# Kernel tuning notes

Hardware: AMD Instinct MI355X
Metric: run time of the kernel (lower is better)

## Reference

```python
import jax, jax.numpy as jnp
import numpy as np

B, D, H, C, HALT_H, MAX_STEPS = 8192, 2048, 1024, 1000, 32, 10
EPS = 1e-08


def setup_inputs() -> dict:
    key = jax.random.key(0)
    ks = jax.random.split(key, 12)
    s = 0.02
    return {
        "x": jax.random.normal(ks[0], (B, D), jnp.float32),
        "enc_W": jax.random.normal(ks[1], (H, D), jnp.float32) * s,
        "enc_b": jnp.zeros((H,), jnp.float32),
        "ln_g": jnp.ones((H,), jnp.float32),
        "ln_b": jnp.zeros((H,), jnp.float32),
        "W_ih": jax.random.normal(ks[2], (3 * H, H), jnp.float32) * s,
        "W_hh": jax.random.normal(ks[3], (3 * H, H), jnp.float32) * s,
        "b_ih": jnp.zeros((3 * H,), jnp.float32),
        "b_hh": jnp.zeros((3 * H,), jnp.float32),
        "cls_W": jax.random.normal(ks[4], (C, H), jnp.float32) * s,
        "cls_b": jnp.zeros((C,), jnp.float32),
        "h1_W": jax.random.normal(ks[5], (HALT_H, H), jnp.float32) * s,
        "h1_b": jnp.zeros((HALT_H,), jnp.float32),
        "h2_W": jax.random.normal(ks[6], (1, HALT_H), jnp.float32) * s,
        "h2_b": jnp.zeros((1,), jnp.float32),
    }


def _forward(x, enc_W, enc_b, ln_g, ln_b, W_ih, W_hh, b_ih, b_hh,
             cls_W, cls_b, h1_W, h1_b, h2_W, h2_b):
    # encoder: Linear -> LayerNorm -> GELU (exact)
    z = x @ enc_W.T + enc_b
    mu = jnp.mean(z, axis=-1, keepdims=True)
    var = jnp.var(z, axis=-1, keepdims=True)
    z = (z - mu) * jax.lax.rsqrt(var + 1e-05) * ln_g + ln_b
    h0 = jax.nn.gelu(z, approximate=False)

    def step(h, _):
        gi = h @ W_ih.T + b_ih   # GRUCell with input = hidden
        gh = h @ W_hh.T + b_hh
        gi_r, gi_z, gi_n = jnp.split(gi, 3, axis=-1)
        gh_r, gh_z, gh_n = jnp.split(gh, 3, axis=-1)
        r = jax.nn.sigmoid(gi_r + gh_r)
        zt = jax.nn.sigmoid(gi_z + gh_z)
        n = jnp.tanh(gi_n + r * gh_n)
        h_new = (1.0 - zt) * n + zt * h
        logits = h_new @ cls_W.T + cls_b                         # [B, C]
        halt = jax.nn.sigmoid(
            jax.nn.relu(h_new @ h1_W.T + h1_b) @ h2_W.T + h2_b
        )[:, 0]                                                   # [B]
        return h_new, (logits, halt)

    _, (logits_steps, halt_steps) = jax.lax.scan(step, h0, None, length=MAX_STEPS)
    logits_stack = jnp.transpose(logits_steps, (1, 0, 2))  # [B, T, C]
    halts_stack = jnp.transpose(halt_steps, (1, 0))        # [B, T]

    log_not_halt = jnp.log(1.0 - halts_stack + EPS)
    cumsum_log = jnp.cumsum(log_not_halt, axis=1)
    cumsum_shifted = jnp.concatenate(
        [jnp.zeros((halts_stack.shape[0], 1), halts_stack.dtype), cumsum_log[:, :-1]], axis=1)
    halt_dist = halts_stack * jnp.exp(cumsum_shifted)
    remainder = 1.0 - jnp.sum(halt_dist, axis=1, keepdims=True)
    halt_dist = jnp.concatenate(
        [halt_dist[:, :-1], halt_dist[:, -1:] + jnp.maximum(remainder, 0.0)], axis=1)

    weighted_logits = jnp.sum(halt_dist[:, :, None] * logits_stack, axis=1)  # [B, C]
    step_indices = jnp.arange(1, MAX_STEPS + 1, dtype=weighted_logits.dtype)
    expected_steps = jnp.sum(halt_dist * step_indices, axis=1)
    probs = jax.nn.softmax(weighted_logits, axis=1)
    softmax_conf = jnp.max(probs, axis=1)
    comp_uncertainty = expected_steps / MAX_STEPS
    confidence = 0.7 * softmax_conf + 0.3 * (1.0 - comp_uncertainty)
    return (weighted_logits, probs, confidence, softmax_conf,
            expected_steps, halt_dist, comp_uncertainty)


def reference(x, enc_W, enc_b, ln_g, ln_b, W_ih, W_hh, b_ih, b_hh,
              cls_W, cls_b, h1_W, h1_b, h2_W, h2_b):
    return _forward(x, enc_W, enc_b, ln_g, ln_b, W_ih, W_hh, b_ih, b_hh,
                    cls_W, cls_b, h1_W, h1_b, h2_W, h2_b)
```

## Files before the change

### kernel.cpp

```cpp
#include <hip/hip_runtime.h>
#include <hip/hip_bf16.h>

#define B_ 8192
#define D_ 2048
#define H_ 1024
#define C_ 1000
#define NSTEP 10

typedef __attribute__((ext_vector_type(8))) short short8;
typedef __attribute__((ext_vector_type(4))) float f32x4;

__device__ __forceinline__ f32x4 mfma16x16(short8 a, short8 b, f32x4 c) {
  return __builtin_amdgcn_mfma_f32_16x16x32_bf16(a, b, c, 0, 0, 0);
}

__device__ __forceinline__ void async16(void* lds_uniform, const void* gsrc) {
  __builtin_amdgcn_global_load_lds(
      (const __attribute__((address_space(1))) void*)gsrc,
      (__attribute__((address_space(3))) void*)lds_uniform, 16, 0, 0);
}

__device__ __forceinline__ float sigm(float x) { return 1.0f / (1.0f + __expf(-x)); }
__device__ __forceinline__ float tanh_fast(float x) { return 1.0f - 2.0f / (__expf(2.0f * x) + 1.0f); }
__device__ __forceinline__ float b2f(short s) {
  union { unsigned u; float f; } v; v.u = ((unsigned)(unsigned short)s) << 16; return v.f;
}
__device__ __forceinline__ unsigned short f2us(float f) {
  __hip_bfloat16 h = __float2bfloat16(f); return *(unsigned short*)&h;
}

__device__ __forceinline__ int swz(int row, int slot) {
  return (row << 7) + (((slot) ^ (row & 7)) << 4);
}

__global__ void cvt_bf16_pad(const float* __restrict__ src, __hip_bfloat16* __restrict__ dst,
                             int n4, int nsrc4) {
  int i = blockIdx.x * 256 + threadIdx.x;
  if (i >= n4) return;
  float4 v = make_float4(0.f, 0.f, 0.f, 0.f);
  if (i < nsrc4) v = ((const float4*)src)[i];
  ((ushort4*)dst)[i] = make_ushort4(f2us(v.x), f2us(v.y), f2us(v.z), f2us(v.w));
}

__global__ void cvt_gates(const float* __restrict__ Wih, const float* __restrict__ Whh,
                          __hip_bfloat16* __restrict__ dst) {
  const int i = blockIdx.x * 256 + threadIdx.x;
  const int per_gate = (H_ * H_) / 4;
  const int gate = i / per_gate, rem = i - gate * per_gate;
  float4 v;
  if (gate == 0) {
    float4 a = ((const float4*)Wih)[rem], b = ((const float4*)Whh)[rem];
    v = make_float4(a.x + b.x, a.y + b.y, a.z + b.z, a.w + b.w);
  } else if (gate == 1) {
    float4 a = ((const float4*)Wih)[per_gate + rem], b = ((const float4*)Whh)[per_gate + rem];
    v = make_float4(a.x + b.x, a.y + b.y, a.z + b.z, a.w + b.w);
  } else if (gate == 2) {
    v = ((const float4*)Wih)[2 * per_gate + rem];
  } else {
    v = ((const float4*)Whh)[2 * per_gate + rem];
  }
  ((ushort4*)dst)[i] = make_ushort4(f2us(v.x), f2us(v.y), f2us(v.z), f2us(v.w));
}

template<int EPI>
__global__ __launch_bounds__(256, 2)
void gemm_bt(const __hip_bfloat16* __restrict__ A, int lda,
             const __hip_bfloat16* __restrict__ Bt, int ldb, int K,
             const float* __restrict__ bias,
             float* __restrict__ out, int out_ld, int ncol,
             const float* __restrict__ wrow) {
  __shared__ __hip_bfloat16 sA[128 * 64];
  __shared__ __hip_bfloat16 sB[128 * 64];
  const int tid = threadIdx.x;
  const int wave = tid >> 6, lane = tid & 63;
  const int m0 = blockIdx.x * 128, n0 = blockIdx.y * 128;
  const int wm = (wave >> 1) * 64, wn = (wave & 1) * 64;
  const int lr = lane & 15;
  const int g4 = lane >> 4;
  const int srow = wave * 8 + (lane >> 3);
  const int scol = ((lane & 7) ^ ((lane >> 3) & 7)) * 8;

  f32x4 acc[4][4] = {};

  const __hip_bfloat16* Asrc = A + (size_t)(m0 + srow) * lda + scol;
  const __hip_bfloat16* Bsrc = Bt + (size_t)(n0 + srow) * ldb + scol;

  for (int k0 = 0; k0 < K; k0 += 64) {
#pragma unroll
    for (int c = 0; c < 4; ++c) {
      async16((char*)sA + c * 4096 + wave * 1024, Asrc + (size_t)(c * 32) * lda + k0);
      async16((char*)sB + c * 4096 + wave * 1024, Bsrc + (size_t)(c * 32) * ldb + k0);
    }
    __syncthreads();
#pragma unroll
    for (int ks = 0; ks < 2; ++ks) {
      const int slot = ks * 4 + g4;
      short8 af[4], bfr[4];
#pragma unroll
      for (int i = 0; i < 4; ++i) {
        af[i]  = *(const short8*)((const char*)sA + swz(wm + i * 16 + lr, slot));
        bfr[i] = *(const short8*)((const char*)sB + swz(wn + i * 16 + lr, slot));
      }
#pragma unroll
      for (int i = 0; i < 4; ++i)
#pragma unroll
        for (int j = 0; j < 4; ++j)
          acc[i][j] = mfma16x16(af[i], bfr[j], acc[i][j]);
    }
    __syncthreads();
  }

  const int rbase = (lane >> 4) * 4;
  const int cbase = lane & 15;
#pragma unroll
  for (int i = 0; i < 4; ++i) {
#pragma unroll
    for (int r = 0; r < 4; ++r) {
      const int grow = m0 + wm + i * 16 + rbase + r;
      if (EPI == 1) {
        const float ws = wrow[grow];
#pragma unroll
        for (int j = 0; j < 4; ++j) {
          const int gcol = n0 + wn + j * 16 + cbase;
          if (gcol < ncol)
            out[(size_t)grow * out_ld + gcol] = acc[i][j][r] + bias[gcol] * ws;
        }
      } else {
#pragma unroll
        for (int j = 0; j < 4; ++j) {
          const int gcol = n0 + wn + j * 16 + cbase;
          out[(size_t)grow * out_ld + gcol] = acc[i][j][r] + bias[gcol];
        }
      }
    }
  }
}

__global__ __launch_bounds__(512, 1)
void gemm_gru(const __hip_bfloat16* __restrict__ A,
              const __hip_bfloat16* __restrict__ Wc4,
              const float* __restrict__ b_ih, const float* __restrict__ b_hh,
              __hip_bfloat16* __restrict__ hnewb) {
  __shared__ __align__(16) char lds[4 * 24576];
  const int tid = threadIdx.x, wave = tid >> 6, lane = tid & 63;
  const int m0 = blockIdx.x * 256, n0 = blockIdx.y * 32;
  const int wm = (wave >> 1) * 64;
  const int wc = wave & 1;
  const int lr = lane & 15, g4 = lane >> 4;
  const int soff = ((g4 ^ ((lr >> 1) & 3)) << 4);

  f32x4 acc[4][4] = {};

  const int scol = (((lane & 3) ^ ((lane >> 3) & 3)) << 3);
  const __hip_bfloat16* AsrcS = A + (size_t)(m0 + wave * 16 + (lane >> 2)) * H_ + scol;
  const __hip_bfloat16* BsrcS = Wc4 + ((size_t)(wave >> 1) << 20)
      + (size_t)(n0 + (wave & 1) * 16 + (lane >> 2)) * H_ + scol;

  auto stageA = [&](char* buf, int kt) {
#pragma unroll
    for (int c = 0; c < 2; ++c)
      async16(buf + c * 8192 + wave * 1024, AsrcS + (size_t)(c * 128) * H_ + kt * 32);
  };
  auto stageB = [&](char* buf, int kt) {
    async16(buf + 16384 + wave * 1024, BsrcS + kt * 32);
  };

  stageA(lds, 0);              stageB(lds, 0);
  stageA(lds + 24576, 1);      stageB(lds + 24576, 1);
  stageA(lds + 2 * 24576, 2);  stageB(lds + 2 * 24576, 2);
  asm volatile("s_waitcnt vmcnt(6)" ::: "memory");
  __builtin_amdgcn_s_barrier();

#pragma unroll 4
  for (int t = 0; t < 32; ++t) {
    char* rb = lds + (t & 3) * 24576;
    char* sb = lds + ((t + 3) & 3) * 24576;
    const bool dostage = (t + 3 < 32);

    short8 af[4], bf01[2];
#pragma unroll
    for (int mi = 0; mi < 4; ++mi)
      af[mi] = *(const short8*)(rb + (wm + mi * 16 + lr) * 64 + soff);
#pragma unroll
    for (int g = 0; g < 2; ++g)
      bf01[g] = *(const short8*)(rb + 16384 + g * 2048 + (wc * 16 + lr) * 64 + soff);
    if (dostage) stageA(sb, t + 3);
    __builtin_amdgcn_s_barrier();
    __builtin_amdgcn_s_setprio(1);
#pragma unroll
    for (int mi = 0; mi < 4; ++mi) {
      acc[mi][0] = mfma16x16(af[mi], bf01[0], acc[mi][0]);
      acc[mi][1] = mfma16x16(af[mi], bf01[1], acc[mi][1]);
    }
    __builtin_amdgcn_s_setprio(0);
    __builtin_amdgcn_s_barrier();

    short8 bf23[2];
#pragma unroll
    for (int g = 0; g < 2; ++g)
      bf23[g] = *(const short8*)(rb + 16384 + (2 + g) * 2048 + (wc * 16 + lr) * 64 + soff);
    if (dostage) stageB(sb, t + 3);
    __builtin_amdgcn_s_barrier();
    __builtin_amdgcn_s_setprio(1);
#pragma unroll
    for (int mi = 0; mi < 4; ++mi) {
      acc[mi][2] = mfma16x16(af[mi], bf23[0], acc[mi][2]);
      acc[mi][3] = mfma16x16(af[mi], bf23[1], acc[mi][3]);
    }
    __builtin_amdgcn_s_setprio(0);
    if (t < 29)       asm volatile("s_waitcnt vmcnt(6)" ::: "memory");
    else if (t == 29) asm volatile("s_waitcnt vmcnt(3)" ::: "memory");
    else if (t == 30) asm volatile("s_waitcnt vmcnt(0)" ::: "memory");
    __builtin_amdgcn_s_barrier();
  }

  const int rbase = (lane >> 4) * 4;
  const int cbase = lane & 15;
  const int gcol = n0 + wc * 16 + cbase;
  const float brz = b_ih[gcol] + b_hh[gcol];
  const float bzz = b_ih[H_ + gcol] + b_hh[H_ + gcol];
  const float bin = b_ih[2 * H_ + gcol];
  const float bhn = b_hh[2 * H_ + gcol];
#pragma unroll
  for (int mi = 0; mi < 4; ++mi) {
#pragma unroll
    for (int r = 0; r < 4; ++r) {
      const int grow = m0 + wm + mi * 16 + rbase + r;
      const size_t idx = (size_t)grow * H_ + gcol;
      const float rg = sigm(acc[mi][0][r] + brz);
      const float zg = sigm(acc[mi][1][r] + bzz);
      const float ng = tanh_fast(acc[mi][2][r] + bin + rg * (acc[mi][3][r] + bhn));
      const float hv = b2f(*(const short*)(A + idx));
      hnewb[idx] = __float2bfloat16((1.0f - zg) * ng + zg * hv);
    }
  }
}

__global__ void ln_gelu(const float* __restrict__ z, const float* __restrict__ g,
                        const float* __restrict__ bta, __hip_bfloat16* __restrict__ hb) {
  const int row = blockIdx.x, t = threadIdx.x;
  __shared__ float rs[4], rs2[4];
  float4 v = ((const float4*)(z + (size_t)row * H_))[t];
  float s = v.x + v.y + v.z + v.w;
  float s2 = v.x * v.x + v.y * v.y + v.z * v.z + v.w * v.w;
#pragma unroll
  for (int off = 32; off; off >>= 1) {
    s += __shfl_down(s, off);
    s2 += __shfl_down(s2, off);
  }
  if ((t & 63) == 0) { rs[t >> 6] = s; rs2[t >> 6] = s2; }
  __syncthreads();
  const float mu = (rs[0] + rs[1] + rs[2] + rs[3]) * (1.0f / H_);
  const float var = (rs2[0] + rs2[1] + rs2[2] + rs2[3]) * (1.0f / H_) - mu * mu;
  const float rstd = rsqrtf(var + 1e-5f);
  float4 gg = ((const float4*)g)[t];
  float4 bb = ((const float4*)bta)[t];
  float o[4], res[4];
  o[0] = (v.x - mu) * rstd * gg.x + bb.x;
  o[1] = (v.y - mu) * rstd * gg.y + bb.y;
  o[2] = (v.z - mu) * rstd * gg.z + bb.z;
  o[3] = (v.w - mu) * rstd * gg.w + bb.w;
#pragma unroll
  for (int k = 0; k < 4; ++k)
    res[k] = 0.5f * o[k] * (1.0f + erff(o[k] * 0.70710678118654752f));
  ((ushort4*)(hb + (size_t)row * H_))[t] =
      make_ushort4(f2us(res[0]), f2us(res[1]), f2us(res[2]), f2us(res[3]));
}

__global__ __launch_bounds__(256, 4)
void halt_mlp2(const __hip_bfloat16* __restrict__ hb,
               const __hip_bfloat16* __restrict__ h1Wb,
               const float* __restrict__ h1b, const float* __restrict__ h2W,
               const float* __restrict__ h2b,
               float* __restrict__ cum, float* __restrict__ psum,
               float* __restrict__ esum, float* __restrict__ wsum,
               float* __restrict__ out_hd, float* __restrict__ out_es,
               float* __restrict__ out_cu, int step) {
  __shared__ float part[2][2][64][8];
  const int tid = threadIdx.x, wave = tid >> 6, lane = tid & 63;
  const int rowgrp = wave >> 1, khalf = wave & 1;
  const int m0 = (blockIdx.x * 2 + rowgrp) * 16;
  const int lr = lane & 15, lk = (lane >> 4) * 8;

  const __hip_bfloat16* Arow = hb + (size_t)(m0 + lr) * H_ + khalf * 512 + lk;
  const __hip_bfloat16* B0 = h1Wb + (size_t)lr * H_ + khalf * 512 + lk;
  const __hip_bfloat16* B1 = h1Wb + (size_t)(16 + lr) * H_ + khalf * 512 + lk;
  f32x4 acc0 = {}, acc1 = {};
#pragma unroll 4
  for (int kk = 0; kk < 512; kk += 32) {
    short8 a  = *(const short8*)(Arow + kk);
    short8 b0 = *(const short8*)(B0 + kk);
    short8 b1 = *(const short8*)(B1 + kk);
    acc0 = mfma16x16(a, b0, acc0);
    acc1 = mfma16x16(a, b1, acc1);
  }
#pragma unroll
  for (int q = 0; q < 4; ++q) {
    part[rowgrp][khalf][lane][q]     = acc0[q];
    part[rowgrp][khalf][lane][4 + q] = acc1[q];
  }
  __syncthreads();
  if (khalf) return;

  const float w2a = h2W[lr], w2b = h2W[16 + lr];
  const float b1a = h1b[lr], b1b = h1b[16 + lr];
  float p[4];
#pragma unroll
  for (int q = 0; q < 4; ++q) {
    const float u0 = part[rowgrp][0][lane][q]     + part[rowgrp][1][lane][q]     + b1a;
    const float u1 = part[rowgrp][0][lane][4 + q] + part[rowgrp][1][lane][4 + q] + b1b;
    p[q] = fmaxf(u0, 0.f) * w2a + fmaxf(u1, 0.f) * w2b;
  }
#pragma unroll
  for (int m = 1; m < 16; m <<= 1) {
#pragma unroll
    for (int q = 0; q < 4; ++q) p[q] += __shfl_xor(p[q], m);
  }
  if (lr == 0) {
    const float b2 = h2b[0];
#pragma unroll
    for (int q = 0; q < 4; ++q) {
      const int rl = (lane >> 4) * 4 + q;
      const int row = m0 + rl;
      const float halt = 1.f / (1.f + expf(-(p[q] + b2)));
      float c  = (step == 0) ? 0.f : cum[row];
      float ps = (step == 0) ? 0.f : psum[row];
      float es = (step == 0) ? 0.f : esum[row];
      const float pt = halt * expf(c);
      float w;
      if (step == NSTEP - 1) {
        w = pt + fmaxf(1.f - (ps + pt), 0.f);
        es += w * (float)NSTEP;
        out_es[row] = es;
        out_cu[row] = es * (1.0f / NSTEP);
        wsum[row] = ps + w;
      } else {
        w = pt;
        es += w * (float)(step + 1);
        cum[row] = c + logf(1.f - halt + 1e-8f);
        psum[row] = ps + pt;
        esum[row] = es;
      }
      out_hd[(size_t)row * NSTEP + step] = w;
    }
  }
}

__global__ void hw_final(const __hip_bfloat16* __restrict__ hstack,
                         const float* __restrict__ out_hd,
                         __hip_bfloat16* __restrict__ hwb) {
  const int t = threadIdx.x;
  const int row = blockIdx.x * 4 + (t >> 6);
  const int c0 = (t & 63) * 16;
  const float* hd = out_hd + (size_t)row * NSTEP;
  float accv[16] = {};
#pragma unroll
  for (int s = 0; s < NSTEP; ++s) {
    const float w = hd[s];
    const short8* p = (const short8*)(hstack + ((size_t)(s + 1) * B_ + row) * H_ + c0);
    short8 a0 = p[0], a1 = p[1];
#pragma unroll
    for (int q = 0; q < 8; ++q) accv[q] += w * b2f(a0[q]);
#pragma unroll
    for (int q = 0; q < 8; ++q) accv[8 + q] += w * b2f(a1[q]);
  }
  short8 r0, r1;
#pragma unroll
  for (int q = 0; q < 8; ++q) { r0[q] = (short)f2us(accv[q]); r1[q] = (short)f2us(accv[8 + q]); }
  short8* dst = (short8*)(hwb + (size_t)row * H_ + c0);
  dst[0] = r0; dst[1] = r1;
}

__global__ void finalize(const float* __restrict__ wl, const float* __restrict__ es,
                         float* __restrict__ probs, float* __restrict__ conf,
                         float* __restrict__ sconf) {
  const int row = blockIdx.x, t = threadIdx.x;
  __shared__ float red[4], red2[4];
  float4 v = make_float4(-1e30f, -1e30f, -1e30f, -1e30f);
  float m = -1e30f;
  if (t < 250) {
    v = ((const float4*)(wl + (size_t)row * C_))[t];
    m = fmaxf(fmaxf(v.x, v.y), fmaxf(v.z, v.w));
  }
#pragma unroll
  for (int off = 32; off; off >>= 1) m = fmaxf(m, __shfl_down(m, off));
  if ((t & 63) == 0) red[t >> 6] = m;
  __syncthreads();
  m = fmaxf(fmaxf(red[0], red[1]), fmaxf(red[2], red[3]));
  float4 e = make_float4(0.f, 0.f, 0.f, 0.f);
  float s = 0.f;
  if (t < 250) {
    e.x = expf(v.x - m); e.y = expf(v.y - m); e.z = expf(v.z - m); e.w = expf(v.w - m);
    s = e.x + e.y + e.z + e.w;
  }
#pragma unroll
  for (int off = 32; off; off >>= 1) s += __shfl_down(s, off);
  if ((t & 63) == 0) red2[t >> 6] = s;
  __syncthreads();
  s = red2[0] + red2[1] + red2[2] + red2[3];
  const float inv = 1.0f / s;
  if (t < 250)
    ((float4*)(probs + (size_t)row * C_))[t] = make_float4(e.x * inv, e.y * inv, e.z * inv, e.w * inv);
  if (t == 0) {
    sconf[row] = inv;
    conf[row] = 0.7f * inv + 0.3f * (1.0f - es[row] * (1.0f / NSTEP));
  }
}

extern "C" void kernel_launch(void* const* d_in, const int* in_sizes, int n_in,
                              void* d_out, int out_size, void* d_ws, size_t ws_size,
                              hipStream_t stream) {
  (void)in_sizes; (void)n_in; (void)out_size; (void)ws_size;
  const float* x     = (const float*)d_in[0];
  const float* enc_W = (const float*)d_in[1];
  const float* enc_b = (const float*)d_in[2];
  const float* ln_g  = (const float*)d_in[3];
  const float* ln_b  = (const float*)d_in[4];
  const float* W_ih  = (const float*)d_in[5];
  const float* W_hh  = (const float*)d_in[6];
  const float* b_ih  = (const float*)d_in[7];
  const float* b_hh  = (const float*)d_in[8];
  const float* cls_W = (const float*)d_in[9];
  const float* cls_b = (const float*)d_in[10];
  const float* h1_W  = (const float*)d_in[11];
  const float* h1_b  = (const float*)d_in[12];
  const float* h2_W  = (const float*)d_in[13];
  const float* h2_b  = (const float*)d_in[14];

  char* wsp = (char*)d_ws;
  auto carve = [&](size_t n) { char* p = wsp; wsp += (n + 255) & ~(size_t)255; return p; };
  __hip_bfloat16* Wc4b   = (__hip_bfloat16*)carve((size_t)4 * H_ * H_ * 2);
  __hip_bfloat16* clsWb  = (__hip_bfloat16*)carve((size_t)1024 * 1024 * 2);
  __hip_bfloat16* encWb  = (__hip_bfloat16*)carve((size_t)H_ * D_ * 2);
  __hip_bfloat16* h1Wb   = (__hip_bfloat16*)carve((size_t)32 * H_ * 2);
  __hip_bfloat16* hstack = (__hip_bfloat16*)carve((size_t)(NSTEP + 1) * B_ * H_ * 2);
  float* cum  = (float*)carve((size_t)B_ * 4);
  float* psum = (float*)carve((size_t)B_ * 4);
  float* esum = (float*)carve((size_t)B_ * 4);
  float* wsum = (float*)carve((size_t)B_ * 4);

  const size_t SLOT = (size_t)B_ * H_;
  float* z            = (float*)(hstack + SLOT);
  __hip_bfloat16* xb  = hstack + 3 * SLOT;
  __hip_bfloat16* hwb = hstack;

  float* out = (float*)d_out;
  float* out_wl    = out;
  float* out_probs = out + (size_t)B_ * C_;
  float* out_conf  = out + (size_t)2 * B_ * C_;
  float* out_sconf = out_conf + B_;
  float* out_es    = out_sconf + B_;
  float* out_hd    = out_es + B_;
  float* out_cu    = out_hd + (size_t)B_ * NSTEP;

  dim3 blk(256);
  { int n4 = B_ * D_ / 4;       cvt_bf16_pad<<<(n4 + 255) / 256, blk, 0, stream>>>(x, xb, n4, n4); }
  { int n4 = H_ * D_ / 4;       cvt_bf16_pad<<<(n4 + 255) / 256, blk, 0, stream>>>(enc_W, encWb, n4, n4); }
  { int n4 = 4 * H_ * H_ / 4;   cvt_gates<<<(n4 + 255) / 256, blk, 0, stream>>>(W_ih, W_hh, Wc4b); }
  { int n4 = 1024 * 1024 / 4;   cvt_bf16_pad<<<(n4 + 255) / 256, blk, 0, stream>>>(cls_W, clsWb, n4, C_ * H_ / 4); }
  { int n4 = 32 * H_ / 4;       cvt_bf16_pad<<<(n4 + 255) / 256, blk, 0, stream>>>(h1_W, h1Wb, n4, n4); }

  gemm_bt<0><<<dim3(B_ / 128, H_ / 128), blk, 0, stream>>>(
      xb, D_, encWb, D_, D_, enc_b, z, H_, H_, nullptr);
  ln_gelu<<<B_, blk, 0, stream>>>(z, ln_g, ln_b, hstack);

  for (int step = 0; step < NSTEP; ++step) {
    const __hip_bfloat16* hprev = hstack + (size_t)step * SLOT;
    __hip_bfloat16* hnext = hstack + (size_t)(step + 1) * SLOT;
    gemm_gru<<<dim3(B_ / 256, H_ / 32), dim3(512), 0, stream>>>(
        hprev, Wc4b, b_ih, b_hh, hnext);
    halt_mlp2<<<B_ / 32, blk, 0, stream>>>(
        hnext, h1Wb, h1_b, h2_W, h2_b, cum, psum, esum, wsum,
        out_hd, out_es, out_cu, step);
  }

  hw_final<<<B_ / 4, blk, 0, stream>>>(hstack, out_hd, hwb);

  gemm_bt<1><<<dim3(B_ / 128, 1024 / 128), blk, 0, stream>>>(
      hwb, H_, clsWb, H_, H_, cls_b, out_wl, C_, C_, wsum);

  finalize<<<B_, blk, 0, stream>>>(out_wl, out_es, out_probs, out_conf, out_sconf);
}
```

Before: 1.082 ms.

## Widen GRU gate GEMM tile to 64 hidden columns per block

Each gemm_gru block now covers 64 hidden columns instead of 32, so every A tile loaded into LDS feeds twice as many MFMAs. The LDS stage buffer grows to 32 KB, B staging issues two loads per wave, and accumulators double to 128 floats per lane. Fragment loads are reorganised so B fragments are held across both A halves, with explicit lgkmcnt waits added. The aim is to cut A-operand global and LDS traffic, at the cost of higher register pressure and half as many blocks in the grid.

```diff
diff --git a/kernel.cpp b/kernel.cpp
--- a/kernel.cpp
+++ b/kernel.cpp
@@ -141,20 +141,21 @@
               const __hip_bfloat16* __restrict__ Wc4,
               const float* __restrict__ b_ih, const float* __restrict__ b_hh,
               __hip_bfloat16* __restrict__ hnewb) {
-  __shared__ __align__(16) char lds[4 * 24576];
+  __shared__ __align__(16) char lds[4 * 32768];
   const int tid = threadIdx.x, wave = tid >> 6, lane = tid & 63;
-  const int m0 = blockIdx.x * 256, n0 = blockIdx.y * 32;
-  const int wm = (wave >> 1) * 64;
+  const int m0 = blockIdx.x * 256, n0 = blockIdx.y * 64;
+  const int wr = wave >> 1;
   const int wc = wave & 1;
+  const int wm = wr * 64;
   const int lr = lane & 15, g4 = lane >> 4;
   const int soff = ((g4 ^ ((lr >> 1) & 3)) << 4);
 
-  f32x4 acc[4][4] = {};
+  f32x4 acc[4][4][2] = {};
 
   const int scol = (((lane & 3) ^ ((lane >> 3) & 3)) << 3);
   const __hip_bfloat16* AsrcS = A + (size_t)(m0 + wave * 16 + (lane >> 2)) * H_ + scol;
-  const __hip_bfloat16* BsrcS = Wc4 + ((size_t)(wave >> 1) << 20)
-      + (size_t)(n0 + (wave & 1) * 16 + (lane >> 2)) * H_ + scol;
+  const __hip_bfloat16* BsrcS = Wc4 + ((size_t)(wave >> 2) << 20)
+      + (size_t)(n0 + (wave & 3) * 16 + (lane >> 2)) * H_ + scol;
 
   auto stageA = [&](char* buf, int kt) {
 #pragma unroll
@@ -162,76 +163,86 @@
       async16(buf + c * 8192 + wave * 1024, AsrcS + (size_t)(c * 128) * H_ + kt * 32);
   };
   auto stageB = [&](char* buf, int kt) {
-    async16(buf + 16384 + wave * 1024, BsrcS + kt * 32);
+#pragma unroll
+    for (int d = 0; d < 2; ++d)
+      async16(buf + 16384 + d * 8192 + wave * 1024, BsrcS + ((size_t)d << 21) + kt * 32);
   };
 
   stageA(lds, 0);              stageB(lds, 0);
-  stageA(lds + 24576, 1);      stageB(lds + 24576, 1);
-  stageA(lds + 2 * 24576, 2);  stageB(lds + 2 * 24576, 2);
-  asm volatile("s_waitcnt vmcnt(6)" ::: "memory");
+  stageA(lds + 32768, 1);      stageB(lds + 32768, 1);
+  stageA(lds + 2 * 32768, 2);  stageB(lds + 2 * 32768, 2);
+  asm volatile("s_waitcnt vmcnt(8)" ::: "memory");
   __builtin_amdgcn_s_barrier();
 
 #pragma unroll 4
   for (int t = 0; t < 32; ++t) {
-    char* rb = lds + (t & 3) * 24576;
-    char* sb = lds + ((t + 3) & 3) * 24576;
-    const bool dostage = (t + 3 < 32);
-
-    short8 af[4], bf01[2];
-#pragma unroll
-    for (int mi = 0; mi < 4; ++mi)
-      af[mi] = *(const short8*)(rb + (wm + mi * 16 + lr) * 64 + soff);
-#pragma unroll
-    for (int g = 0; g < 2; ++g)
-      bf01[g] = *(const short8*)(rb + 16384 + g * 2048 + (wc * 16 + lr) * 64 + soff);
+    char* rb = lds + (t & 3) * 32768;
+    char* sb = lds + ((t + 3) & 3) * 32768;
+    const bool dostage = (t < 29);
+
+    short8 af0 = *(const short8*)(rb + (wm + 0 * 16 + lr) * 64 + soff);
+    short8 af1 = *(const short8*)(rb + (wm + 1 * 16 + lr) * 64 + soff);
+    short8 bf[4][2];
+#pragma unroll
+    for (int g = 0; g < 4; ++g)
+#pragma unroll
+      for (int hb = 0; hb < 2; ++hb)
+        bf[g][hb] = *(const short8*)(rb + 16384 + (g * 64 + wc * 32 + hb * 16 + lr) * 64 + soff);
     if (dostage) stageA(sb, t + 3);
     __builtin_amdgcn_s_barrier();
+    asm volatile("s_waitcnt lgkmcnt(0)" ::: "memory");
     __builtin_amdgcn_s_setprio(1);
 #pragma unroll
-    for (int mi = 0; mi < 4; ++mi) {
-      acc[mi][0] = mfma16x16(af[mi], bf01[0], acc[mi][0]);
-      acc[mi][1] = mfma16x16(af[mi], bf01[1], acc[mi][1]);
-    }
+    for (int g = 0; g < 4; ++g)
+#pragma unroll
+      for (int hb = 0; hb < 2; ++hb) {
+        acc[0][g][hb] = mfma16x16(af0, bf[g][hb], acc[0][g][hb]);
+        acc[1][g][hb] = mfma16x16(af1, bf[g][hb], acc[1][g][hb]);
+      }
     __builtin_amdgcn_s_setprio(0);
     __builtin_amdgcn_s_barrier();
 
-    short8 bf23[2];
-#pragma unroll
-    for (int g = 0; g < 2; ++g)
-      bf23[g] = *(const short8*)(rb + 16384 + (2 + g) * 2048 + (wc * 16 + lr) * 64 + soff);
+    short8 af2 = *(const short8*)(rb + (wm + 2 * 16 + lr) * 64 + soff);
+    short8 af3 = *(const short8*)(rb + (wm + 3 * 16 + lr) * 64 + soff);
     if (dostage) stageB(sb, t + 3);
     __builtin_amdgcn_s_barrier();
+    asm volatile("s_waitcnt lgkmcnt(0)" ::: "memory");
     __builtin_amdgcn_s_setprio(1);
 #pragma unroll
-    for (int mi = 0; mi < 4; ++mi) {
-      acc[mi][2] = mfma16x16(af[mi], bf23[0], acc[mi][2]);
-      acc[mi][3] = mfma16x16(af[mi], bf23[1], acc[mi][3]);
-    }
+    for (int g = 0; g < 4; ++g)
+#pragma unroll
+      for (int hb = 0; hb < 2; ++hb) {
+        acc[2][g][hb] = mfma16x16(af2, bf[g][hb], acc[2][g][hb]);
+        acc[3][g][hb] = mfma16x16(af3, bf[g][hb], acc[3][g][hb]);
+      }
     __builtin_amdgcn_s_setprio(0);
-    if (t < 29)       asm volatile("s_waitcnt vmcnt(6)" ::: "memory");
-    else if (t == 29) asm volatile("s_waitcnt vmcnt(3)" ::: "memory");
+    if (t < 29)       asm volatile("s_waitcnt vmcnt(8)" ::: "memory");
+    else if (t == 29) asm volatile("s_waitcnt vmcnt(4)" ::: "memory");
     else if (t == 30) asm volatile("s_waitcnt vmcnt(0)" ::: "memory");
     __builtin_amdgcn_s_barrier();
   }
 
   const int rbase = (lane >> 4) * 4;
   const int cbase = lane & 15;
-  const int gcol = n0 + wc * 16 + cbase;
-  const float brz = b_ih[gcol] + b_hh[gcol];
-  const float bzz = b_ih[H_ + gcol] + b_hh[H_ + gcol];
-  const float bin = b_ih[2 * H_ + gcol];
-  const float bhn = b_hh[2 * H_ + gcol];
-#pragma unroll
-  for (int mi = 0; mi < 4; ++mi) {
-#pragma unroll
-    for (int r = 0; r < 4; ++r) {
-      const int grow = m0 + wm + mi * 16 + rbase + r;
-      const size_t idx = (size_t)grow * H_ + gcol;
-      const float rg = sigm(acc[mi][0][r] + brz);
-      const float zg = sigm(acc[mi][1][r] + bzz);
-      const float ng = tanh_fast(acc[mi][2][r] + bin + rg * (acc[mi][3][r] + bhn));
-      const float hv = b2f(*(const short*)(A + idx));
-      hnewb[idx] = __float2bfloat16((1.0f - zg) * ng + zg * hv);
+#pragma unroll
+  for (int hb = 0; hb < 2; ++hb) {
+    const int gcol = n0 + wc * 32 + hb * 16 + cbase;
+    const float brz = b_ih[gcol] + b_hh[gcol];
+    const float bzz = b_ih[H_ + gcol] + b_hh[H_ + gcol];
+    const float bin = b_ih[2 * H_ + gcol];
+    const float bhn = b_hh[2 * H_ + gcol];
+#pragma unroll
+    for (int mi = 0; mi < 4; ++mi) {
+#pragma unroll
+      for (int r = 0; r < 4; ++r) {
+        const int grow = m0 + wm + mi * 16 + rbase + r;
+        const size_t idx = (size_t)grow * H_ + gcol;
+        const float rg = sigm(acc[mi][0][hb][r] + brz);
+        const float zg = sigm(acc[mi][1][hb][r] + bzz);
+        const float ng = tanh_fast(acc[mi][2][hb][r] + bin + rg * (acc[mi][3][hb][r] + bhn));
+        const float hv = b2f(*(const short*)(A + idx));
+        hnewb[idx] = __float2bfloat16((1.0f - zg) * ng + zg * hv);
+      }
     }
   }
 }
@@ -467,7 +478,7 @@
   for (int step = 0; step < NSTEP; ++step) {
     const __hip_bfloat16* hprev = hstack + (size_t)step * SLOT;
     __hip_bfloat16* hnext = hstack + (size_t)(step + 1) * SLOT;
-    gemm_gru<<<dim3(B_ / 256, H_ / 32), dim3(512), 0, stream>>>(
+    gemm_gru<<<dim3(B_ / 256, H_ / 64), dim3(512), 0, stream>>>(
         hprev, Wc4b, b_ih, b_hh, hnext);
     halt_mlp2<<<B_ / 32, blk, 0, stream>>>(
         hnext, h1Wb, h1_b, h2_W, h2_b, cum, psum, esum, wsum,
```

Result: faster. 997.2 us (-7.9%).
